# Optimization experiments

Hardware: AMD Instinct MI355X
Metric: run time of the kernel (lower is better)

## Reference

```python
import jax, jax.numpy as jnp
import numpy as np

# NAM: in_features independent 1->H->H->1 MLPs (FeatureNNs), batched over the
# feature dimension F instead of a Python loop of tiny kernels.
# inputs: (B, F); W1,b1: (F, H); W2: (F, H, H); b2: (F, H); W3: (F, H); b3: (F,)

def setup_inputs() -> dict:
    key = jax.random.key(0)
    ks = jax.random.split(key, 7)
    B, F, H = 8192, 128, 64
    s1 = 1.0  # fan_in = 1 for first layer
    s2 = 1.0 / np.sqrt(H)
    return {
        "inputs": jax.random.normal(ks[0], (B, F), dtype=jnp.float32),
        "W1": jax.random.normal(ks[1], (F, H), dtype=jnp.float32) * s1,
        "b1": jax.random.normal(ks[2], (F, H), dtype=jnp.float32) * 0.01,
        "W2": jax.random.normal(ks[3], (F, H, H), dtype=jnp.float32) * s2,
        "b2": jax.random.normal(ks[4], (F, H), dtype=jnp.float32) * 0.01,
        "W3": jax.random.normal(ks[5], (F, H), dtype=jnp.float32) * s2,
        "b3": jax.random.normal(ks[6], (F,), dtype=jnp.float32) * 0.01,
    }


def reference(inputs, W1, b1, W2, b2, W3, b3):
    # Layer 1: scalar input per feature -> hidden.  (B,F,1)*(F,H) -> (B,F,H)
    h1 = jax.nn.relu(inputs[:, :, None] * W1[None, :, :] + b1[None, :, :])
    # Layer 2: per-feature hidden->hidden batched matmul.
    h2 = jax.nn.relu(jnp.einsum("bfh,fhk->bfk", h1, W2) + b2[None, :, :])
    # Output layer: hidden -> scalar per feature.
    fnn = jnp.einsum("bfh,fh->bf", h2, W3) + b3[None, :]  # (B, F)
    out = fnn.sum(axis=-1)  # (B,)  additive model output
    return (out, fnn)
```

## Files before the change

kernel.cpp:

```cpp
#include <hip/hip_runtime.h>

#define B 8192
#define F 128
#define H 64

typedef __attribute__((ext_vector_type(8))) short bf16x8;
typedef __attribute__((ext_vector_type(4))) float f32x4;

static __device__ __forceinline__ unsigned short f32_to_bf16_rne(float v) {
    unsigned int u = __float_as_uint(v);
    unsigned int r = (u + 0x7FFFu + ((u >> 16) & 1u)) >> 16;
    return (unsigned short)r;
}
static __device__ __forceinline__ float bf16_to_f32(unsigned short h) {
    return __uint_as_float(((unsigned int)h) << 16);
}

__global__ __launch_bounds__(256, 3) void nam_main(
    const float* __restrict__ inputs, const float* __restrict__ W1,
    const float* __restrict__ b1, const float* __restrict__ W2,
    const float* __restrict__ b2, const float* __restrict__ W3,
    const float* __restrict__ b3, float* __restrict__ out,
    float* __restrict__ fnn_out)
{
    const int tid = threadIdx.x;
    const int f = blockIdx.y;
    const int b0 = blockIdx.x * 256;

    const float* W1f = W1 + f * H;
    const float* b1f = b1 + f * H;
    const float* W2f = W2 + (size_t)f * H * H;
    const float* b2f = b2 + f * H;
    const float* W3f = W3 + f * H;

    __shared__ short bhi_s[512 * 8];
    __shared__ short blo_s[512 * 8];

#pragma unroll
    for (int t = tid; t < 512; t += 256) {
        const int n = t & 63;
        const int g = t >> 6;
        const int nt = n >> 4, c = n & 15;
        const int ks = g >> 2, q = g & 3;
        const int slot = (nt * 2 + ks) * 64 + c + 16 * q;
        bf16x8 hv, lv;
#pragma unroll
        for (int jj = 0; jj < 8; ++jj) {
            const float wv = W2f[(g * 8 + jj) * H + n];
            const unsigned short hi = f32_to_bf16_rne(wv);
            const unsigned short lo = f32_to_bf16_rne(wv - bf16_to_f32(hi));
            hv[jj] = (short)hi;
            lv[jj] = (short)lo;
        }
        *(bf16x8*)&bhi_s[slot * 8] = hv;
        *(bf16x8*)&blo_s[slot * 8] = lv;
    }

    const int lane = tid & 63;
    const int w    = tid >> 6;
    const int q    = lane >> 4;
    const int col  = lane & 15;

    float w1v[16], b1v[16];
#pragma unroll
    for (int ks = 0; ks < 2; ++ks)
#pragma unroll
        for (int j = 0; j < 8; ++j) {
            w1v[ks * 8 + j] = W1f[ks * 32 + q * 8 + j];
            b1v[ks * 8 + j] = b1f[ks * 32 + q * 8 + j];
        }
    float b2v[4], w3v[4];
#pragma unroll
    for (int nt = 0; nt < 4; ++nt) {
        b2v[nt] = b2f[nt * 16 + col];
        w3v[nt] = W3f[nt * 16 + col];
    }
    const float b3f = b3[f];

    float x4[4];
#pragma unroll
    for (int mt = 0; mt < 4; ++mt)
        x4[mt] = inputs[(size_t)(b0 + w * 64 + mt * 16 + col) * F + f];

    __syncthreads();

    bf16x8 bhi[4][2], blo[4][2];
#pragma unroll
    for (int nt = 0; nt < 4; ++nt)
#pragma unroll
        for (int ks = 0; ks < 2; ++ks) {
            const int slot = (nt * 2 + ks) * 64 + lane;
            bhi[nt][ks] = *(bf16x8*)&bhi_s[slot * 8];
            blo[nt][ks] = *(bf16x8*)&blo_s[slot * 8];
        }

#pragma unroll 1
    for (int mt = 0; mt < 4; ++mt) {
        const int rbase = b0 + w * 64 + mt * 16;
        const float x = x4[mt];

        f32x4 acc[4];
#pragma unroll
        for (int nt = 0; nt < 4; ++nt) {
            acc[nt][0] = b2v[nt]; acc[nt][1] = b2v[nt];
            acc[nt][2] = b2v[nt]; acc[nt][3] = b2v[nt];
        }

#pragma unroll
        for (int ks = 0; ks < 2; ++ks) {
            union { unsigned int u[4]; bf16x8 v; } Ah, Al;
#pragma unroll
            for (int t = 0; t < 4; ++t) {
                const float r0 = fmaxf(fmaf(x, w1v[ks * 8 + 2 * t],     b1v[ks * 8 + 2 * t]),     0.0f);
                const float r1 = fmaxf(fmaf(x, w1v[ks * 8 + 2 * t + 1], b1v[ks * 8 + 2 * t + 1]), 0.0f);
                const unsigned int u0 = __float_as_uint(r0);
                const unsigned int u1 = __float_as_uint(r1);
                const float l0 = r0 - __uint_as_float(u0 & 0xFFFF0000u);
                const float l1 = r1 - __uint_as_float(u1 & 0xFFFF0000u);
                Ah.u[t] = __builtin_amdgcn_perm(u1, u0, 0x07060302);
                Al.u[t] = __builtin_amdgcn_perm(__float_as_uint(l1),
                                                __float_as_uint(l0), 0x07060302);
            }
#pragma unroll
            for (int nt = 0; nt < 4; ++nt) {
                acc[nt] = __builtin_amdgcn_mfma_f32_16x16x32_bf16(Ah.v, bhi[nt][ks], acc[nt], 0, 0, 0);
                acc[nt] = __builtin_amdgcn_mfma_f32_16x16x32_bf16(Ah.v, blo[nt][ks], acc[nt], 0, 0, 0);
                acc[nt] = __builtin_amdgcn_mfma_f32_16x16x32_bf16(Al.v, bhi[nt][ks], acc[nt], 0, 0, 0);
            }
        }

        float s[4];
#pragma unroll
        for (int reg = 0; reg < 4; ++reg) {
            float t = 0.0f;
#pragma unroll
            for (int nt = 0; nt < 4; ++nt)
                t = fmaf(fmaxf(acc[nt][reg], 0.0f), w3v[nt], t);
            s[reg] = t;
        }
#pragma unroll
        for (int m_ = 1; m_ <= 8; m_ <<= 1)
#pragma unroll
            for (int reg = 0; reg < 4; ++reg)
                s[reg] += __shfl_xor(s[reg], m_, 64);
        if (col == 0) {
#pragma unroll
            for (int reg = 0; reg < 4; ++reg) {
                const int row = rbase + 4 * q + reg;
                const float val = s[reg] + b3f;
                fnn_out[(size_t)row * F + f] = val;
                atomicAdd(&out[row], val);
            }
        }
    }
}

extern "C" void kernel_launch(void* const* d_in, const int* in_sizes, int n_in,
                              void* d_out, int out_size, void* d_ws, size_t ws_size,
                              hipStream_t stream) {
    const float* inputs = (const float*)d_in[0];
    const float* W1     = (const float*)d_in[1];
    const float* b1     = (const float*)d_in[2];
    const float* W2     = (const float*)d_in[3];
    const float* b2     = (const float*)d_in[4];
    const float* W3     = (const float*)d_in[5];
    const float* b3     = (const float*)d_in[6];

    float* out = (float*)d_out;
    float* fnn = out + B;

    hipMemsetAsync(out, 0, B * sizeof(float), stream);
    nam_main<<<dim3(B / 256, F), 256, 0, stream>>>(inputs, W1, b1, W2, b2, W3,
                                                   b3, out, fnn);
}
```

Measured before the change: 107.7 us.

## Prepack W2 hi/lo bf16 fragments once into workspace, drop per-block LDS staging

Adds a separate kernel that converts each feature's W2 into hi/lo bf16 MFMA fragments once and writes them to the workspace. The main kernel then loads those fragments straight from global memory into registers, so it no longer needs LDS staging, the __syncthreads, or the conversion that each of the 32 batch blocks per feature used to repeat. The mt loop is now fully unrolled and W1/b1 are read with float4 loads. The cost is an extra kernel launch plus about 2 MB of workspace traffic. Occupancy drops to launch bounds 2, and the old LDS path is kept as a fallback for when the workspace is too small.

```diff
diff --git a/kernel.cpp b/kernel.cpp
--- a/kernel.cpp
+++ b/kernel.cpp
@@ -16,9 +16,37 @@
     return __uint_as_float(((unsigned int)h) << 16);
 }
 
-__global__ __launch_bounds__(256, 3) void nam_main(
+
+__global__ __launch_bounds__(256) void w2_pack(const float* __restrict__ W2,
+                                               bf16x8* __restrict__ ws)
+{
+    const int f = blockIdx.x;
+    const int tid = threadIdx.x;
+    const float* W2f = W2 + (size_t)f * H * H;
+#pragma unroll
+    for (int t = tid; t < 512; t += 256) {
+        const int n = t & 63;
+        const int g = t >> 6;
+        const int nt = n >> 4, c = n & 15;
+        const int ks = g >> 2, q = g & 3;
+        const int slot = (nt * 2 + ks) * 64 + c + 16 * q;
+        bf16x8 hv, lv;
+#pragma unroll
+        for (int jj = 0; jj < 8; ++jj) {
+            const float wv = W2f[(g * 8 + jj) * H + n];
+            const unsigned short hi = f32_to_bf16_rne(wv);
+            const unsigned short lo = f32_to_bf16_rne(wv - bf16_to_f32(hi));
+            hv[jj] = (short)hi;
+            lv[jj] = (short)lo;
+        }
+        ws[((size_t)f * 2 + 0) * 512 + slot] = hv;
+        ws[((size_t)f * 2 + 1) * 512 + slot] = lv;
+    }
+}
+
+__global__ __launch_bounds__(256, 2) void nam_main_ws(
     const float* __restrict__ inputs, const float* __restrict__ W1,
-    const float* __restrict__ b1, const float* __restrict__ W2,
+    const float* __restrict__ b1, const bf16x8* __restrict__ wsb,
     const float* __restrict__ b2, const float* __restrict__ W3,
     const float* __restrict__ b3, float* __restrict__ out,
     float* __restrict__ fnn_out)
@@ -27,47 +55,37 @@
     const int f = blockIdx.y;
     const int b0 = blockIdx.x * 256;
 
-    const float* W1f = W1 + f * H;
-    const float* b1f = b1 + f * H;
-    const float* W2f = W2 + (size_t)f * H * H;
-    const float* b2f = b2 + f * H;
-    const float* W3f = W3 + f * H;
-
-    __shared__ short bhi_s[512 * 8];
-    __shared__ short blo_s[512 * 8];
-
-#pragma unroll
-    for (int t = tid; t < 512; t += 256) {
-        const int n = t & 63;
-        const int g = t >> 6;
-        const int nt = n >> 4, c = n & 15;
-        const int ks = g >> 2, q = g & 3;
-        const int slot = (nt * 2 + ks) * 64 + c + 16 * q;
-        bf16x8 hv, lv;
-#pragma unroll
-        for (int jj = 0; jj < 8; ++jj) {
-            const float wv = W2f[(g * 8 + jj) * H + n];
-            const unsigned short hi = f32_to_bf16_rne(wv);
-            const unsigned short lo = f32_to_bf16_rne(wv - bf16_to_f32(hi));
-            hv[jj] = (short)hi;
-            lv[jj] = (short)lo;
-        }
-        *(bf16x8*)&bhi_s[slot * 8] = hv;
-        *(bf16x8*)&blo_s[slot * 8] = lv;
-    }
-
     const int lane = tid & 63;
     const int w    = tid >> 6;
     const int q    = lane >> 4;
     const int col  = lane & 15;
 
+    bf16x8 bhi[4][2], blo[4][2];
+#pragma unroll
+    for (int nt = 0; nt < 4; ++nt)
+#pragma unroll
+        for (int ks = 0; ks < 2; ++ks) {
+            const int slot = (nt * 2 + ks) * 64 + lane;
+            bhi[nt][ks] = wsb[((size_t)f * 2 + 0) * 512 + slot];
+            blo[nt][ks] = wsb[((size_t)f * 2 + 1) * 512 + slot];
+        }
+
+    const float* W1f = W1 + f * H;
+    const float* b1f = b1 + f * H;
+    const float* b2f = b2 + f * H;
+    const float* W3f = W3 + f * H;
+
     float w1v[16], b1v[16];
 #pragma unroll
     for (int ks = 0; ks < 2; ++ks)
 #pragma unroll
-        for (int j = 0; j < 8; ++j) {
-            w1v[ks * 8 + j] = W1f[ks * 32 + q * 8 + j];
-            b1v[ks * 8 + j] = b1f[ks * 32 + q * 8 + j];
+        for (int j4 = 0; j4 < 2; ++j4) {
+            const float4 wv = *(const float4*)&W1f[ks * 32 + q * 8 + j4 * 4];
+            const float4 bv = *(const float4*)&b1f[ks * 32 + q * 8 + j4 * 4];
+            w1v[ks * 8 + j4 * 4 + 0] = wv.x; w1v[ks * 8 + j4 * 4 + 1] = wv.y;
+            w1v[ks * 8 + j4 * 4 + 2] = wv.z; w1v[ks * 8 + j4 * 4 + 3] = wv.w;
+            b1v[ks * 8 + j4 * 4 + 0] = bv.x; b1v[ks * 8 + j4 * 4 + 1] = bv.y;
+            b1v[ks * 8 + j4 * 4 + 2] = bv.z; b1v[ks * 8 + j4 * 4 + 3] = bv.w;
         }
     float b2v[4], w3v[4];
 #pragma unroll
@@ -82,19 +100,7 @@
     for (int mt = 0; mt < 4; ++mt)
         x4[mt] = inputs[(size_t)(b0 + w * 64 + mt * 16 + col) * F + f];
 
-    __syncthreads();
-
-    bf16x8 bhi[4][2], blo[4][2];
-#pragma unroll
-    for (int nt = 0; nt < 4; ++nt)
-#pragma unroll
-        for (int ks = 0; ks < 2; ++ks) {
-            const int slot = (nt * 2 + ks) * 64 + lane;
-            bhi[nt][ks] = *(bf16x8*)&bhi_s[slot * 8];
-            blo[nt][ks] = *(bf16x8*)&blo_s[slot * 8];
-        }
-
-#pragma unroll 1
+#pragma unroll
     for (int mt = 0; mt < 4; ++mt) {
         const int rbase = b0 + w * 64 + mt * 16;
         const float x = x4[mt];
@@ -155,6 +161,140 @@
     }
 }
 
+__global__ __launch_bounds__(256, 3) void nam_main_lds(
+    const float* __restrict__ inputs, const float* __restrict__ W1,
+    const float* __restrict__ b1, const float* __restrict__ W2,
+    const float* __restrict__ b2, const float* __restrict__ W3,
+    const float* __restrict__ b3, float* __restrict__ out,
+    float* __restrict__ fnn_out)
+{
+    const int tid = threadIdx.x;
+    const int f = blockIdx.y;
+    const int b0 = blockIdx.x * 256;
+
+    const float* W1f = W1 + f * H;
+    const float* b1f = b1 + f * H;
+    const float* W2f = W2 + (size_t)f * H * H;
+    const float* b2f = b2 + f * H;
+    const float* W3f = W3 + f * H;
+
+    __shared__ short bhi_s[512 * 8];
+    __shared__ short blo_s[512 * 8];
+
+#pragma unroll
+    for (int t = tid; t < 512; t += 256) {
+        const int n = t & 63, g = t >> 6;
+        const int nt = n >> 4, c = n & 15;
+        const int ks = g >> 2, q = g & 3;
+        const int slot = (nt * 2 + ks) * 64 + c + 16 * q;
+        bf16x8 hv, lv;
+#pragma unroll
+        for (int jj = 0; jj < 8; ++jj) {
+            const float wv = W2f[(g * 8 + jj) * H + n];
+            const unsigned short hi = f32_to_bf16_rne(wv);
+            const unsigned short lo = f32_to_bf16_rne(wv - bf16_to_f32(hi));
+            hv[jj] = (short)hi;
+            lv[jj] = (short)lo;
+        }
+        *(bf16x8*)&bhi_s[slot * 8] = hv;
+        *(bf16x8*)&blo_s[slot * 8] = lv;
+    }
+
+    const int lane = tid & 63, w = tid >> 6;
+    const int q = lane >> 4, col = lane & 15;
+
+    float w1v[16], b1v[16];
+#pragma unroll
+    for (int ks = 0; ks < 2; ++ks)
+#pragma unroll
+        for (int j = 0; j < 8; ++j) {
+            w1v[ks * 8 + j] = W1f[ks * 32 + q * 8 + j];
+            b1v[ks * 8 + j] = b1f[ks * 32 + q * 8 + j];
+        }
+    float b2v[4], w3v[4];
+#pragma unroll
+    for (int nt = 0; nt < 4; ++nt) {
+        b2v[nt] = b2f[nt * 16 + col];
+        w3v[nt] = W3f[nt * 16 + col];
+    }
+    const float b3f = b3[f];
+
+    float x4[4];
+#pragma unroll
+    for (int mt = 0; mt < 4; ++mt)
+        x4[mt] = inputs[(size_t)(b0 + w * 64 + mt * 16 + col) * F + f];
+
+    __syncthreads();
+
+    bf16x8 bhi[4][2], blo[4][2];
+#pragma unroll
+    for (int nt = 0; nt < 4; ++nt)
+#pragma unroll
+        for (int ks = 0; ks < 2; ++ks) {
+            const int slot = (nt * 2 + ks) * 64 + lane;
+            bhi[nt][ks] = *(bf16x8*)&bhi_s[slot * 8];
+            blo[nt][ks] = *(bf16x8*)&blo_s[slot * 8];
+        }
+
+#pragma unroll 1
+    for (int mt = 0; mt < 4; ++mt) {
+        const int rbase = b0 + w * 64 + mt * 16;
+        const float x = x4[mt];
+
+        f32x4 acc[4];
+#pragma unroll
+        for (int nt = 0; nt < 4; ++nt) {
+            acc[nt][0] = b2v[nt]; acc[nt][1] = b2v[nt];
+            acc[nt][2] = b2v[nt]; acc[nt][3] = b2v[nt];
+        }
+#pragma unroll
+        for (int ks = 0; ks < 2; ++ks) {
+            union { unsigned int u[4]; bf16x8 v; } Ah, Al;
+#pragma unroll
+            for (int t = 0; t < 4; ++t) {
+                const float r0 = fmaxf(fmaf(x, w1v[ks * 8 + 2 * t],     b1v[ks * 8 + 2 * t]),     0.0f);
+                const float r1 = fmaxf(fmaf(x, w1v[ks * 8 + 2 * t + 1], b1v[ks * 8 + 2 * t + 1]), 0.0f);
+                const unsigned int u0 = __float_as_uint(r0);
+                const unsigned int u1 = __float_as_uint(r1);
+                const float l0 = r0 - __uint_as_float(u0 & 0xFFFF0000u);
+                const float l1 = r1 - __uint_as_float(u1 & 0xFFFF0000u);
+                Ah.u[t] = __builtin_amdgcn_perm(u1, u0, 0x07060302);
+                Al.u[t] = __builtin_amdgcn_perm(__float_as_uint(l1),
+                                                __float_as_uint(l0), 0x07060302);
+            }
+#pragma unroll
+            for (int nt = 0; nt < 4; ++nt) {
+                acc[nt] = __builtin_amdgcn_mfma_f32_16x16x32_bf16(Ah.v, bhi[nt][ks], acc[nt], 0, 0, 0);
+                acc[nt] = __builtin_amdgcn_mfma_f32_16x16x32_bf16(Ah.v, blo[nt][ks], acc[nt], 0, 0, 0);
+                acc[nt] = __builtin_amdgcn_mfma_f32_16x16x32_bf16(Al.v, bhi[nt][ks], acc[nt], 0, 0, 0);
+            }
+        }
+        float s[4];
+#pragma unroll
+        for (int reg = 0; reg < 4; ++reg) {
+            float t = 0.0f;
+#pragma unroll
+            for (int nt = 0; nt < 4; ++nt)
+                t = fmaf(fmaxf(acc[nt][reg], 0.0f), w3v[nt], t);
+            s[reg] = t;
+        }
+#pragma unroll
+        for (int m_ = 1; m_ <= 8; m_ <<= 1)
+#pragma unroll
+            for (int reg = 0; reg < 4; ++reg)
+                s[reg] += __shfl_xor(s[reg], m_, 64);
+        if (col == 0) {
+#pragma unroll
+            for (int reg = 0; reg < 4; ++reg) {
+                const int row = rbase + 4 * q + reg;
+                const float val = s[reg] + b3f;
+                fnn_out[(size_t)row * F + f] = val;
+                atomicAdd(&out[row], val);
+            }
+        }
+    }
+}
+
 extern "C" void kernel_launch(void* const* d_in, const int* in_sizes, int n_in,
                               void* d_out, int out_size, void* d_ws, size_t ws_size,
                               hipStream_t stream) {
@@ -170,6 +310,15 @@
     float* fnn = out + B;
 
     hipMemsetAsync(out, 0, B * sizeof(float), stream);
-    nam_main<<<dim3(B / 256, F), 256, 0, stream>>>(inputs, W1, b1, W2, b2, W3,
-                                                   b3, out, fnn);
-}
+
+    const size_t ws_needed = (size_t)F * 2 * 512 * sizeof(bf16x8);
+    if (ws_size >= ws_needed) {
+        bf16x8* wsb = (bf16x8*)d_ws;
+        w2_pack<<<dim3(F), 256, 0, stream>>>(W2, wsb);
+        nam_main_ws<<<dim3(B / 256, F), 256, 0, stream>>>(
+            inputs, W1, b1, wsb, b2, W3, b3, out, fnn);
+    } else {
+        nam_main_lds<<<dim3(B / 256, F), 256, 0, stream>>>(
+            inputs, W1, b1, W2, b2, W3, b3, out, fnn);
+    }
+}
```

Result: slower. 113.8 us (+5.6%).
